# Performance work log

Measured on AMD Instinct MI355X. Metric: run time of the kernel, lower is better.

## Reference

```python
import jax, jax.numpy as jnp
import numpy as np

B, S, D = 16, 2048, 128


def setup_inputs() -> dict:
    k = jax.random.key(0)
    k1, k2, k3, k4 = jax.random.split(k, 4)
    query = jax.random.normal(k1, (B, S, D), dtype=jnp.float32)
    key = jax.random.normal(k2, (B, S, D), dtype=jnp.float32)
    value = jax.random.normal(k3, (B, S, D), dtype=jnp.float32)
    # per-query tensor-valued inverse scale; shift away from zero for stable division
    inv_scale_factor = jax.random.uniform(k4, (B, S, 1), dtype=jnp.float32) + 0.5
    dropout_p = jnp.float32(0.1)
    return {"query": query, "key": key, "value": value,
            "inv_scale_factor": inv_scale_factor, "dropout_p": dropout_p}


def reference(query, key, value, inv_scale_factor, dropout_p):
    # QK^T: [B, Sq, Sk]
    qk = jnp.einsum('bqd,bkd->bqk', query, key)
    # tensor-valued scale divide (broadcast [B, Sq, 1] over keys)
    scaled_qk = qk / inv_scale_factor
    softmax_qk = jax.nn.softmax(scaled_qk, axis=-1)
    # dropout with a fixed RNG key (deterministic reference)
    keep_prob = 1.0 - dropout_p
    mask = jax.random.bernoulli(jax.random.key(42), keep_prob, softmax_qk.shape)
    dropout_qk = jnp.where(mask, softmax_qk / keep_prob, jnp.float32(0.0))
    # AV: [B, Sq, Dv]
    return jnp.einsum('bqk,bkv->bqv', dropout_qk, value)
```

## Files before the change

kernel.cpp:

```cpp
#include <hip/hip_runtime.h>
#include <stdint.h>


#define B_ 16
#define S_ 2048
#define D_ 128
#define TQ 64
#define TK 64
#define NT (S_ / TK)
#define KSTR 136
#define VSTR 72
#define PSTR 40

typedef float f32x4 __attribute__((ext_vector_type(4)));
typedef _Float16 f16x8 __attribute__((ext_vector_type(8)));
typedef _Float16 f16x2 __attribute__((ext_vector_type(2)));

union F32R8 { float4 q[8]; float f[32]; };

#define DPP_ROR(x, ctrl) \
  __int_as_float(__builtin_amdgcn_update_dpp(0, __float_as_int(x), (ctrl), 0xf, 0xf, true))
__device__ __forceinline__ float row16_max(float x) {
  x = fmaxf(x, DPP_ROR(x, 0x128));
  x = fmaxf(x, DPP_ROR(x, 0x124));
  x = fmaxf(x, DPP_ROR(x, 0x122));
  x = fmaxf(x, DPP_ROR(x, 0x121));
  return x;
}
__device__ __forceinline__ float row16_sum(float x) {
  x += DPP_ROR(x, 0x128);
  x += DPP_ROR(x, 0x124);
  x += DPP_ROR(x, 0x122);
  x += DPP_ROR(x, 0x121);
  return x;
}

__device__ __forceinline__ uint2 threefry2x32_0_42(uint32_t x0, uint32_t x1) {
  const uint32_t k0 = 0u, k1 = 42u;
  const uint32_t k2 = 0x1BD11BDAu ^ k0 ^ k1;
  x0 += k0; x1 += k1;
#define TFR(r) { x0 += x1; x1 = __builtin_rotateleft32(x1, r); x1 ^= x0; }
  TFR(13) TFR(15) TFR(26) TFR(6)
  x0 += k1; x1 += k2 + 1u;
  TFR(17) TFR(29) TFR(16) TFR(24)
  x0 += k2; x1 += k0 + 2u;
  TFR(13) TFR(15) TFR(26) TFR(6)
  x0 += k0; x1 += k1 + 3u;
  TFR(17) TFR(29) TFR(16) TFR(24)
  x0 += k1; x1 += k2 + 4u;
  TFR(13) TFR(15) TFR(26) TFR(6)
  x0 += k2; x1 += k0 + 5u;
#undef TFR
  return make_uint2(x0, x1);
}

__device__ __forceinline__ uint32_t jax_bits(uint32_t j) {
  const uint2 tf = threefry2x32_0_42(0u, j);
  return tf.x ^ tf.y;
}

__global__ __launch_bounds__(256, 2)
void attn_mfma_kernel(const float* __restrict__ Q, const float* __restrict__ K,
                      const float* __restrict__ V, const float* __restrict__ ISF,
                      const float* __restrict__ DP, float* __restrict__ OUT) {
  extern __shared__ __align__(16) char smem[];
  _Float16* const sK0  = (_Float16*)smem;
  _Float16* const sK1  = (_Float16*)(smem + 17408);
  _Float16* const sVT0 = (_Float16*)(smem + 34816);
  _Float16* const sVT1 = (_Float16*)(smem + 53248);
  _Float16* const sP   = (_Float16*)(smem + 71680);
  float* const sO1 = (float*)smem;
  float* const sM1 = (float*)(smem + 32768);
  float* const sL1 = (float*)(smem + 33024);

  const int t    = threadIdx.x;
  const int lane = t & 63;
  const int l15  = lane & 15;
  const int quad = lane >> 4;
  const int w    = t >> 6;
  const int qg   = w & 1;
  const int kph  = w >> 1;
  const int b    = blockIdx.y;
  const int qb   = blockIdx.x * TQ + qg * 32;

  const float kp = 1.0f - DP[0];
  const uint32_t TH9 = (__float_as_uint(1.0f + kp) & 0x7FFFFFu) << 9;

  float m_[2][4], l_[2][4];
  uint32_t jq[2][4];
  #pragma unroll
  for (int sub = 0; sub < 2; ++sub)
    #pragma unroll
    for (int r = 0; r < 4; ++r) {
      m_[sub][r] = -INFINITY;
      l_[sub][r] = 0.0f;
      jq[sub][r] = ((uint32_t)b << 22)
                 + (uint32_t)(qb + sub * 16 + quad * 4 + r) * (uint32_t)S_;
    }

  f16x8 qf[2][4];
  #pragma unroll
  for (int sub = 0; sub < 2; ++sub) {
    const int qrow = qb + sub * 16 + l15;
    const float qs = 1.4426950408889634f / ISF[b * S_ + qrow];
    const float* qp = Q + ((size_t)(b * S_ + qrow)) * D_;
    #pragma unroll
    for (int c = 0; c < 4; ++c) {
      const float4 a  = *(const float4*)(qp + c * 32 + quad * 8);
      const float4 d2 = *(const float4*)(qp + c * 32 + quad * 8 + 4);
      const float xs[8] = {a.x, a.y, a.z, a.w, d2.x, d2.y, d2.z, d2.w};
      f16x8 h;
      #pragma unroll
      for (int j = 0; j < 8; ++j) h[j] = (_Float16)(xs[j] * qs);
      qf[sub][c] = h;
    }
  }

  f32x4 accO[2][8];
  #pragma unroll
  for (int sub = 0; sub < 2; ++sub)
    #pragma unroll
    for (int i = 0; i < 8; ++i) accO[sub][i] = (f32x4){0.f, 0.f, 0.f, 0.f};

  _Float16* const pwv = &sP[w * 32 * PSTR];

  const int krow = t >> 2, kcol = (t & 3) * 32;
  const int vp = t & 31, dseg = (t >> 5) * 16;

  F32R8 kreg;
  F32R8 vreg;

#define ISSUE_LOADS(KT)                                                        \
  {                                                                            \
    const float4* gk4 = (const float4*)(K +                                    \
        ((size_t)(b * S_ + (KT) * TK + krow)) * D_ + kcol);                    \
    _Pragma("unroll") for (int i = 0; i < 8; ++i) kreg.q[i] = gk4[i];          \
    const float4* gv4 = (const float4*)(V +                                    \
        ((size_t)(b * S_ + (KT) * TK + 2 * vp)) * D_ + dseg);                  \
    _Pragma("unroll") for (int i = 0; i < 4; ++i) {                            \
      vreg.q[i] = gv4[i];                                                      \
      vreg.q[i + 4] = gv4[i + 32];             \
    }                                                                          \
  }

#define CONVERT_TO(KB, VB)                                                     \
  {                                                                            \
    _Pragma("unroll") for (int g = 0; g < 4; ++g) {                            \
      f16x8 h;                                                                 \
      _Pragma("unroll") for (int j = 0; j < 8; ++j)                            \
        h[j] = (_Float16)kreg.f[g * 8 + j];                                    \
      *(f16x8*)&(KB)[krow * KSTR + kcol + g * 8] = h;                          \
    }                                                                          \
    _Pragma("unroll") for (int d = 0; d < 16; ++d) {                           \
      f16x2 h = {(_Float16)vreg.f[d], (_Float16)vreg.f[16 + d]};               \
      *(f16x2*)&(VB)[(dseg + d) * VSTR + 2 * vp] = h;                          \
    }                                                                          \
  }

  ISSUE_LOADS(0)
  CONVERT_TO(sK0, sVT0)
  ISSUE_LOADS(1)
  __syncthreads();

  for (int kt = 0; kt < NT; ++kt) {
    const int cur = kt & 1;
    _Float16* const sKc = cur ? sK1 : sK0;
    _Float16* const sVc = cur ? sVT1 : sVT0;

    f32x4 s[2][2];
    #pragma unroll
    for (int n = 0; n < 2; ++n) {
      f32x4 a0 = (f32x4){0.f, 0.f, 0.f, 0.f};
      f32x4 a1 = (f32x4){0.f, 0.f, 0.f, 0.f};
      #pragma unroll
      for (int c = 0; c < 4; ++c) {
        const f16x8 bh = *(const f16x8*)&sKc[(kph * 32 + n * 16 + l15) * KSTR
                                             + c * 32 + quad * 8];
        a0 = __builtin_amdgcn_mfma_f32_16x16x32_f16(qf[0][c], bh, a0, 0, 0, 0);
        a1 = __builtin_amdgcn_mfma_f32_16x16x32_f16(qf[1][c], bh, a1, 0, 0, 0);
      }
      s[0][n] = a0;
      s[1][n] = a1;
    }

    uint32_t rb[2][2][4];
    #pragma unroll
    for (int sub = 0; sub < 2; ++sub)
      #pragma unroll
      for (int n = 0; n < 2; ++n) {
        const uint32_t jcol = (uint32_t)(kt * TK + kph * 32 + n * 16 + l15);
        #pragma unroll
        for (int r = 0; r < 4; ++r)
          rb[sub][n][r] = jax_bits(jq[sub][r] + jcol);
      }

    float mx[2][4];
    int changed = 0;
    #pragma unroll
    for (int sub = 0; sub < 2; ++sub)
      #pragma unroll
      for (int r = 0; r < 4; ++r) {
        mx[sub][r] = row16_max(fmaxf(s[sub][0][r], s[sub][1][r]));
        changed |= (mx[sub][r] > m_[sub][r]);
      }
    if (__ballot(changed) != 0ull) {
      #pragma unroll
      for (int sub = 0; sub < 2; ++sub)
        #pragma unroll
        for (int r = 0; r < 4; ++r) {
          const float mnew = fmaxf(m_[sub][r], mx[sub][r]);
          const float alpha = __builtin_amdgcn_exp2f(m_[sub][r] - mnew);
          m_[sub][r] = mnew;
          l_[sub][r] *= alpha;
          #pragma unroll
          for (int i = 0; i < 8; ++i) accO[sub][i][r] *= alpha;
        }
    }
    #pragma unroll
    for (int sub = 0; sub < 2; ++sub)
      #pragma unroll
      for (int r = 0; r < 4; ++r) {
        const float p0 = __builtin_amdgcn_exp2f(s[sub][0][r] - m_[sub][r]);
        const float p1 = __builtin_amdgcn_exp2f(s[sub][1][r] - m_[sub][r]);
        s[sub][0][r] = p0;
        s[sub][1][r] = p1;
        l_[sub][r] += row16_sum(p0 + p1);
      }

    #pragma unroll
    for (int sub = 0; sub < 2; ++sub)
      #pragma unroll
      for (int n = 0; n < 2; ++n) {
        const int col = n * 16 + l15;
        #pragma unroll
        for (int r = 0; r < 4; ++r) {
          const float pf = (rb[sub][n][r] < TH9) ? s[sub][n][r] : 0.0f;
          pwv[(sub * 16 + quad * 4 + r) * PSTR + col] = (_Float16)pf;
        }
      }
    __threadfence_block();

    {
      const f16x8 ap0 = *(const f16x8*)&pwv[l15 * PSTR + quad * 8];
      const f16x8 ap1 = *(const f16x8*)&pwv[(16 + l15) * PSTR + quad * 8];
      #pragma unroll
      for (int d8 = 0; d8 < 8; ++d8) {
        const f16x8 bv = *(const f16x8*)&sVc[(d8 * 16 + l15) * VSTR
                                             + kph * 32 + quad * 8];
        accO[0][d8] = __builtin_amdgcn_mfma_f32_16x16x32_f16(ap0, bv, accO[0][d8], 0, 0, 0);
        accO[1][d8] = __builtin_amdgcn_mfma_f32_16x16x32_f16(ap1, bv, accO[1][d8], 0, 0, 0);
      }
    }

    if (kt + 1 < NT) {
      _Float16* const sKn = cur ? sK0 : sK1;
      _Float16* const sVn = cur ? sVT0 : sVT1;
      CONVERT_TO(sKn, sVn)
      if (kt + 2 < NT) ISSUE_LOADS(kt + 2)
    }
    __syncthreads();
  }
#undef ISSUE_LOADS
#undef CONVERT_TO

  if (kph == 1) {
    #pragma unroll
    for (int sub = 0; sub < 2; ++sub) {
      if (l15 == 0) {
        #pragma unroll
        for (int r = 0; r < 4; ++r) {
          const int gr = qg * 32 + sub * 16 + quad * 4 + r;
          sM1[gr] = m_[sub][r];
          sL1[gr] = l_[sub][r];
        }
      }
      #pragma unroll
      for (int d8 = 0; d8 < 8; ++d8)
        #pragma unroll
        for (int r = 0; r < 4; ++r) {
          const int gr = qg * 32 + sub * 16 + quad * 4 + r;
          sO1[gr * D_ + d8 * 16 + l15] = accO[sub][d8][r];
        }
    }
  }
  __syncthreads();
  if (kph == 0) {
    #pragma unroll
    for (int sub = 0; sub < 2; ++sub) {
      float a0s[4], a1s[4];
      #pragma unroll
      for (int r = 0; r < 4; ++r) {
        const int gr = qg * 32 + sub * 16 + quad * 4 + r;
        const float m1  = sM1[gr];
        const float l1v = sL1[gr];
        const float mf = fmaxf(m_[sub][r], m1);
        const float a0 = __builtin_amdgcn_exp2f(m_[sub][r] - mf);
        const float a1 = __builtin_amdgcn_exp2f(m1 - mf);
        const float inv = 1.0f / ((a0 * l_[sub][r] + a1 * l1v) * kp);
        a0s[r] = a0 * inv;
        a1s[r] = a1 * inv;
      }
      #pragma unroll
      for (int d8 = 0; d8 < 8; ++d8)
        #pragma unroll
        for (int r = 0; r < 4; ++r) {
          const int gr = qg * 32 + sub * 16 + quad * 4 + r;
          const float o1 = sO1[gr * D_ + d8 * 16 + l15];
          OUT[((size_t)(b * S_ + blockIdx.x * TQ + gr)) * D_ + d8 * 16 + l15] =
              accO[sub][d8][r] * a0s[r] + o1 * a1s[r];
        }
    }
  }
}

extern "C" void kernel_launch(void* const* d_in, const int* in_sizes, int n_in,
                              void* d_out, int out_size, void* d_ws, size_t ws_size,
                              hipStream_t stream) {
  const float* q   = (const float*)d_in[0];
  const float* k   = (const float*)d_in[1];
  const float* v   = (const float*)d_in[2];
  const float* isf = (const float*)d_in[3];
  const float* dp  = (const float*)d_in[4];
  float* out = (float*)d_out;

  dim3 grid(S_ / TQ, B_);
  attn_mfma_kernel<<<grid, dim3(256), 81920, stream>>>(q, k, v, isf, dp, out);
}
```

Measured before the change: 310.8 us.

## Split work across 8 waves with 16-row query tiles and lazy rescaling

The block grows from 256 to 512 threads, so each wave handles one 16-row query sub-tile instead of two. This halves per-thread accumulator, Q-fragment and load registers, and doubles the waves hiding latency and the threefry RNG work. The online-softmax rescale now fires only when the row max grows by more than 8 (log2 units). The per-iteration row sum reduction is deferred to a single DPP reduction at the end. Fewer iterations pay the rescale and cross-lane reductions, at the cost of less Q-fragment reuse per K load and more waves contending for LDS and barriers.

Measured after the change: 329.8 us. +6.1%, slower.

```diff
diff --git a/kernel.cpp b/kernel.cpp
--- a/kernel.cpp
+++ b/kernel.cpp
@@ -16,7 +16,7 @@
 typedef _Float16 f16x8 __attribute__((ext_vector_type(8)));
 typedef _Float16 f16x2 __attribute__((ext_vector_type(2)));
 
-union F32R8 { float4 q[8]; float f[32]; };
+union F32R4 { float4 q[4]; float f[16]; };
 
 #define DPP_ROR(x, ctrl) \
   __int_as_float(__builtin_amdgcn_update_dpp(0, __float_as_int(x), (ctrl), 0xf, 0xf, true))
@@ -59,7 +59,7 @@
   return tf.x ^ tf.y;
 }
 
-__global__ __launch_bounds__(256, 2)
+__global__ __launch_bounds__(512, 3)
 void attn_mfma_kernel(const float* __restrict__ Q, const float* __restrict__ K,
                       const float* __restrict__ V, const float* __restrict__ ISF,
                       const float* __restrict__ DP, float* __restrict__ OUT) {
@@ -78,30 +78,27 @@
   const int l15  = lane & 15;
   const int quad = lane >> 4;
   const int w    = t >> 6;
-  const int qg   = w & 1;
-  const int kph  = w >> 1;
+  const int qsub = w >> 1;
+  const int kph  = w & 1;
   const int b    = blockIdx.y;
-  const int qb   = blockIdx.x * TQ + qg * 32;
+  const int qb   = blockIdx.x * TQ + qsub * 16;
 
   const float kp = 1.0f - DP[0];
   const uint32_t TH9 = (__float_as_uint(1.0f + kp) & 0x7FFFFFu) << 9;
 
-  float m_[2][4], l_[2][4];
-  uint32_t jq[2][4];
+  float m_[4], l_[4];
+  uint32_t jq[4];
   #pragma unroll
-  for (int sub = 0; sub < 2; ++sub)
-    #pragma unroll
-    for (int r = 0; r < 4; ++r) {
-      m_[sub][r] = -INFINITY;
-      l_[sub][r] = 0.0f;
-      jq[sub][r] = ((uint32_t)b << 22)
-                 + (uint32_t)(qb + sub * 16 + quad * 4 + r) * (uint32_t)S_;
-    }
-
-  f16x8 qf[2][4];
-  #pragma unroll
-  for (int sub = 0; sub < 2; ++sub) {
-    const int qrow = qb + sub * 16 + l15;
+  for (int r = 0; r < 4; ++r) {
+    m_[r] = -INFINITY;
+    l_[r] = 0.0f;
+    jq[r] = ((uint32_t)b << 22)
+          + (uint32_t)(qb + quad * 4 + r) * (uint32_t)S_;
+  }
+
+  f16x8 qf[4];
+  {
+    const int qrow = qb + l15;
     const float qs = 1.4426950408889634f / ISF[b * S_ + qrow];
     const float* qp = Q + ((size_t)(b * S_ + qrow)) * D_;
     #pragma unroll
@@ -112,47 +109,45 @@
       f16x8 h;
       #pragma unroll
       for (int j = 0; j < 8; ++j) h[j] = (_Float16)(xs[j] * qs);
-      qf[sub][c] = h;
-    }
-  }
-
-  f32x4 accO[2][8];
+      qf[c] = h;
+    }
+  }
+
+  f32x4 accO[8];
   #pragma unroll
-  for (int sub = 0; sub < 2; ++sub)
-    #pragma unroll
-    for (int i = 0; i < 8; ++i) accO[sub][i] = (f32x4){0.f, 0.f, 0.f, 0.f};
-
-  _Float16* const pwv = &sP[w * 32 * PSTR];
-
-  const int krow = t >> 2, kcol = (t & 3) * 32;
-  const int vp = t & 31, dseg = (t >> 5) * 16;
-
-  F32R8 kreg;
-  F32R8 vreg;
+  for (int i = 0; i < 8; ++i) accO[i] = (f32x4){0.f, 0.f, 0.f, 0.f};
+
+  _Float16* const pwv = &sP[w * 16 * PSTR];
+
+  const int krow = t >> 3, kcol = (t & 7) * 16;
+  const int vp = t & 31, dseg = (t >> 5) * 8;
+
+  F32R4 kreg;
+  F32R4 vreg;
 
 #define ISSUE_LOADS(KT)                                                        \
   {                                                                            \
     const float4* gk4 = (const float4*)(K +                                    \
         ((size_t)(b * S_ + (KT) * TK + krow)) * D_ + kcol);                    \
-    _Pragma("unroll") for (int i = 0; i < 8; ++i) kreg.q[i] = gk4[i];          \
+    _Pragma("unroll") for (int i = 0; i < 4; ++i) kreg.q[i] = gk4[i];          \
     const float4* gv4 = (const float4*)(V +                                    \
         ((size_t)(b * S_ + (KT) * TK + 2 * vp)) * D_ + dseg);                  \
-    _Pragma("unroll") for (int i = 0; i < 4; ++i) {                            \
+    _Pragma("unroll") for (int i = 0; i < 2; ++i) {                            \
       vreg.q[i] = gv4[i];                                                      \
-      vreg.q[i + 4] = gv4[i + 32];             \
+      vreg.q[i + 2] = gv4[i + 32];             \
     }                                                                          \
   }
 
 #define CONVERT_TO(KB, VB)                                                     \
   {                                                                            \
-    _Pragma("unroll") for (int g = 0; g < 4; ++g) {                            \
+    _Pragma("unroll") for (int g = 0; g < 2; ++g) {                            \
       f16x8 h;                                                                 \
       _Pragma("unroll") for (int j = 0; j < 8; ++j)                            \
         h[j] = (_Float16)kreg.f[g * 8 + j];                                    \
       *(f16x8*)&(KB)[krow * KSTR + kcol + g * 8] = h;                          \
     }                                                                          \
-    _Pragma("unroll") for (int d = 0; d < 16; ++d) {                           \
-      f16x2 h = {(_Float16)vreg.f[d], (_Float16)vreg.f[16 + d]};               \
+    _Pragma("unroll") for (int d = 0; d < 8; ++d) {                            \
+      f16x2 h = {(_Float16)vreg.f[d], (_Float16)vreg.f[8 + d]};                \
       *(f16x2*)&(VB)[(dseg + d) * VSTR + 2 * vp] = h;                          \
     }                                                                          \
   }
@@ -167,88 +162,73 @@
     _Float16* const sKc = cur ? sK1 : sK0;
     _Float16* const sVc = cur ? sVT1 : sVT0;
 
-    f32x4 s[2][2];
+    f32x4 s[2];
     #pragma unroll
     for (int n = 0; n < 2; ++n) {
       f32x4 a0 = (f32x4){0.f, 0.f, 0.f, 0.f};
-      f32x4 a1 = (f32x4){0.f, 0.f, 0.f, 0.f};
       #pragma unroll
       for (int c = 0; c < 4; ++c) {
         const f16x8 bh = *(const f16x8*)&sKc[(kph * 32 + n * 16 + l15) * KSTR
                                              + c * 32 + quad * 8];
-        a0 = __builtin_amdgcn_mfma_f32_16x16x32_f16(qf[0][c], bh, a0, 0, 0, 0);
-        a1 = __builtin_amdgcn_mfma_f32_16x16x32_f16(qf[1][c], bh, a1, 0, 0, 0);
-      }
-      s[0][n] = a0;
-      s[1][n] = a1;
-    }
-
-    uint32_t rb[2][2][4];
-    #pragma unroll
-    for (int sub = 0; sub < 2; ++sub)
-      #pragma unroll
-      for (int n = 0; n < 2; ++n) {
-        const uint32_t jcol = (uint32_t)(kt * TK + kph * 32 + n * 16 + l15);
+        a0 = __builtin_amdgcn_mfma_f32_16x16x32_f16(qf[c], bh, a0, 0, 0, 0);
+      }
+      s[n] = a0;
+    }
+
+    uint32_t rb[2][4];
+    #pragma unroll
+    for (int n = 0; n < 2; ++n) {
+      const uint32_t jcol = (uint32_t)(kt * TK + kph * 32 + n * 16 + l15);
+      #pragma unroll
+      for (int r = 0; r < 4; ++r)
+        rb[n][r] = jax_bits(jq[r] + jcol);
+    }
+
+    float mx[4];
+    int changed = 0;
+    #pragma unroll
+    for (int r = 0; r < 4; ++r) {
+      mx[r] = row16_max(fmaxf(s[0][r], s[1][r]));
+      changed |= (mx[r] > m_[r] + 8.0f);
+    }
+    if (__ballot(changed) != 0ull) {
+      #pragma unroll
+      for (int r = 0; r < 4; ++r) {
+        const float mnew = fmaxf(m_[r], mx[r]);
+        const float alpha = __builtin_amdgcn_exp2f(m_[r] - mnew);
+        m_[r] = mnew;
+        l_[r] *= alpha;
         #pragma unroll
-        for (int r = 0; r < 4; ++r)
-          rb[sub][n][r] = jax_bits(jq[sub][r] + jcol);
-      }
-
-    float mx[2][4];
-    int changed = 0;
-    #pragma unroll
-    for (int sub = 0; sub < 2; ++sub)
-      #pragma unroll
-      for (int r = 0; r < 4; ++r) {
-        mx[sub][r] = row16_max(fmaxf(s[sub][0][r], s[sub][1][r]));
-        changed |= (mx[sub][r] > m_[sub][r]);
-      }
-    if (__ballot(changed) != 0ull) {
-      #pragma unroll
-      for (int sub = 0; sub < 2; ++sub)
-        #pragma unroll
-        for (int r = 0; r < 4; ++r) {
-          const float mnew = fmaxf(m_[sub][r], mx[sub][r]);
-          const float alpha = __builtin_amdgcn_exp2f(m_[sub][r] - mnew);
-          m_[sub][r] = mnew;
-          l_[sub][r] *= alpha;
-          #pragma unroll
-          for (int i = 0; i < 8; ++i) accO[sub][i][r] *= alpha;
-        }
-    }
-    #pragma unroll
-    for (int sub = 0; sub < 2; ++sub)
-      #pragma unroll
-      for (int r = 0; r < 4; ++r) {
-        const float p0 = __builtin_amdgcn_exp2f(s[sub][0][r] - m_[sub][r]);
-        const float p1 = __builtin_amdgcn_exp2f(s[sub][1][r] - m_[sub][r]);
-        s[sub][0][r] = p0;
-        s[sub][1][r] = p1;
-        l_[sub][r] += row16_sum(p0 + p1);
-      }
-
-    #pragma unroll
-    for (int sub = 0; sub < 2; ++sub)
-      #pragma unroll
-      for (int n = 0; n < 2; ++n) {
-        const int col = n * 16 + l15;
-        #pragma unroll
-        for (int r = 0; r < 4; ++r) {
-          const float pf = (rb[sub][n][r] < TH9) ? s[sub][n][r] : 0.0f;
-          pwv[(sub * 16 + quad * 4 + r) * PSTR + col] = (_Float16)pf;
-        }
-      }
+        for (int i = 0; i < 8; ++i) accO[i][r] *= alpha;
+      }
+    }
+    #pragma unroll
+    for (int r = 0; r < 4; ++r) {
+      const float p0 = __builtin_amdgcn_exp2f(s[0][r] - m_[r]);
+      const float p1 = __builtin_amdgcn_exp2f(s[1][r] - m_[r]);
+      s[0][r] = p0;
+      s[1][r] = p1;
+      l_[r] += p0 + p1;
+    }
+
+    #pragma unroll
+    for (int n = 0; n < 2; ++n) {
+      const int col = n * 16 + l15;
+      #pragma unroll
+      for (int r = 0; r < 4; ++r) {
+        const float pf = (rb[n][r] < TH9) ? s[n][r] : 0.0f;
+        pwv[(quad * 4 + r) * PSTR + col] = (_Float16)pf;
+      }
+    }
     __threadfence_block();
 
     {
-      const f16x8 ap0 = *(const f16x8*)&pwv[l15 * PSTR + quad * 8];
-      const f16x8 ap1 = *(const f16x8*)&pwv[(16 + l15) * PSTR + quad * 8];
+      const f16x8 ap = *(const f16x8*)&pwv[l15 * PSTR + quad * 8];
       #pragma unroll
       for (int d8 = 0; d8 < 8; ++d8) {
         const f16x8 bv = *(const f16x8*)&sVc[(d8 * 16 + l15) * VSTR
                                              + kph * 32 + quad * 8];
-        accO[0][d8] = __builtin_amdgcn_mfma_f32_16x16x32_f16(ap0, bv, accO[0][d8], 0, 0, 0);
-        accO[1][d8] = __builtin_amdgcn_mfma_f32_16x16x32_f16(ap1, bv, accO[1][d8], 0, 0, 0);
+        accO[d8] = __builtin_amdgcn_mfma_f32_16x16x32_f16(ap, bv, accO[d8], 0, 0, 0);
       }
     }
 
@@ -263,53 +243,51 @@
 #undef ISSUE_LOADS
 #undef CONVERT_TO
 
+  #pragma unroll
+  for (int r = 0; r < 4; ++r)
+    l_[r] = row16_sum(l_[r]);
+
   if (kph == 1) {
-    #pragma unroll
-    for (int sub = 0; sub < 2; ++sub) {
-      if (l15 == 0) {
-        #pragma unroll
-        for (int r = 0; r < 4; ++r) {
-          const int gr = qg * 32 + sub * 16 + quad * 4 + r;
-          sM1[gr] = m_[sub][r];
-          sL1[gr] = l_[sub][r];
-        }
-      }
-      #pragma unroll
-      for (int d8 = 0; d8 < 8; ++d8)
-        #pragma unroll
-        for (int r = 0; r < 4; ++r) {
-          const int gr = qg * 32 + sub * 16 + quad * 4 + r;
-          sO1[gr * D_ + d8 * 16 + l15] = accO[sub][d8][r];
-        }
-    }
+    if (l15 == 0) {
+      #pragma unroll
+      for (int r = 0; r < 4; ++r) {
+        const int gr = qsub * 16 + quad * 4 + r;
+        sM1[gr] = m_[r];
+        sL1[gr] = l_[r];
+      }
+    }
+    #pragma unroll
+    for (int d8 = 0; d8 < 8; ++d8)
+      #pragma unroll
+      for (int r = 0; r < 4; ++r) {
+        const int gr = qsub * 16 + quad * 4 + r;
+        sO1[gr * D_ + d8 * 16 + l15] = accO[d8][r];
+      }
   }
   __syncthreads();
   if (kph == 0) {
-    #pragma unroll
-    for (int sub = 0; sub < 2; ++sub) {
-      float a0s[4], a1s[4];
-      #pragma unroll
-      for (int r = 0; r < 4; ++r) {
-        const int gr = qg * 32 + sub * 16 + quad * 4 + r;
-        const float m1  = sM1[gr];
-        const float l1v = sL1[gr];
-        const float mf = fmaxf(m_[sub][r], m1);
-        const float a0 = __builtin_amdgcn_exp2f(m_[sub][r] - mf);
-        const float a1 = __builtin_amdgcn_exp2f(m1 - mf);
-        const float inv = 1.0f / ((a0 * l_[sub][r] + a1 * l1v) * kp);
-        a0s[r] = a0 * inv;
-        a1s[r] = a1 * inv;
-      }
-      #pragma unroll
-      for (int d8 = 0; d8 < 8; ++d8)
-        #pragma unroll
-        for (int r = 0; r < 4; ++r) {
-          const int gr = qg * 32 + sub * 16 + quad * 4 + r;
-          const float o1 = sO1[gr * D_ + d8 * 16 + l15];
-          OUT[((size_t)(b * S_ + blockIdx.x * TQ + gr)) * D_ + d8 * 16 + l15] =
-              accO[sub][d8][r] * a0s[r] + o1 * a1s[r];
-        }
-    }
+    float a0s[4], a1s[4];
+    #pragma unroll
+    for (int r = 0; r < 4; ++r) {
+      const int gr = qsub * 16 + quad * 4 + r;
+      const float m1  = sM1[gr];
+      const float l1v = sL1[gr];
+      const float mf = fmaxf(m_[r], m1);
+      const float a0 = __builtin_amdgcn_exp2f(m_[r] - mf);
+      const float a1 = __builtin_amdgcn_exp2f(m1 - mf);
+      const float inv = 1.0f / ((a0 * l_[r] + a1 * l1v) * kp);
+      a0s[r] = a0 * inv;
+      a1s[r] = a1 * inv;
+    }
+    #pragma unroll
+    for (int d8 = 0; d8 < 8; ++d8)
+      #pragma unroll
+      for (int r = 0; r < 4; ++r) {
+        const int gr = qsub * 16 + quad * 4 + r;
+        const float o1 = sO1[gr * D_ + d8 * 16 + l15];
+        OUT[((size_t)(b * S_ + blockIdx.x * TQ + gr)) * D_ + d8 * 16 + l15] =
+            accO[d8][r] * a0s[r] + o1 * a1s[r];
+      }
   }
 }
 
@@ -324,5 +302,5 @@
   float* out = (float*)d_out;
 
   dim3 grid(S_ / TQ, B_);
-  attn_mfma_kernel<<<grid, dim3(256), 81920, stream>>>(q, k, v, isf, dp, out);
-}
+  attn_mfma_kernel<<<grid, dim3(512), 81920, stream>>>(q, k, v, isf, dp, out);
+}
```
